# Optimization experiments

Measured on AMD Instinct MI355X. Metric: run time of the kernel, lower is better.

The kernel has to match this reference:

```python
import jax, jax.numpy as jnp
import numpy as np

HEADS = 16
D_MODEL = 1024
D_EXP = 2048  # d_model * expansion_factor
D_HEAD = D_EXP // HEADS
DEPTH = 12
B, L = 2, 2048


def setup_inputs() -> dict:
    key = jax.random.key(0)
    ks = jax.random.split(key, 4)
    x = jax.random.normal(ks[0], (B, L, D_MODEL), dtype=jnp.float32)
    w_in = jax.random.normal(ks[1], (4 * D_EXP, D_MODEL), dtype=jnp.float32) * 0.02
    w_out = jax.random.normal(ks[2], (D_MODEL, D_EXP), dtype=jnp.float32) * (0.02 / np.sqrt(2 * DEPTH))
    # LearnedALiBi init: logspace(0,-6,heads//2,base=2) ++ zeros(heads - heads//2)
    half = HEADS // 2
    slopes = jnp.concatenate([
        jnp.asarray(2.0 ** np.linspace(0.0, -6.0, half), dtype=jnp.float32),
        jnp.zeros((HEADS - half,), dtype=jnp.float32),
    ])
    smear_factor = jnp.linspace(-6.0, 6.0, HEADS, dtype=jnp.float32)
    return {
        "x": x, "w_in": w_in, "w_out": w_out,
        "ln_in_g": jnp.ones((D_MODEL,), jnp.float32), "ln_in_b": jnp.zeros((D_MODEL,), jnp.float32),
        "ln_out_g": jnp.ones((D_MODEL,), jnp.float32), "ln_out_b": jnp.zeros((D_MODEL,), jnp.float32),
        "slopes": slopes, "smear_factor": smear_factor,
    }


def _layernorm(x, g, b, eps=1e-5):
    mu = jnp.mean(x, axis=-1, keepdims=True)
    var = jnp.mean(jnp.square(x - mu), axis=-1, keepdims=True)
    return (x - mu) * jax.lax.rsqrt(var + eps) * g + b


def reference(x, w_in, w_out, ln_in_g, ln_in_b, ln_out_g, ln_out_b, slopes, smear_factor):
    b, l, d = x.shape
    h = _layernorm(x, ln_in_g, ln_in_b)
    qkvp = h @ w_in.T  # (b, l, 4*D_EXP)
    q, k, v, p = jnp.split(qkvp, 4, axis=-1)

    def to_heads(t):  # b i (h d) -> b h i d
        return t.reshape(b, l, HEADS, D_HEAD).transpose(0, 2, 1, 3)

    q, k, v = to_heads(q), to_heads(k), to_heads(v)

    # key smearing: k_i <- (1-s)*k_i + s*k_{i-1}
    smear = jax.nn.sigmoid(smear_factor)[None, :, None, None]
    k_shift = jnp.pad(k, ((0, 0), (0, 0), (1, 0), (0, 0)))[:, :, :-1]
    k = (1.0 - smear) * k + smear * k_shift

    logits = jnp.einsum('bhid,bhjd->bhij', q, k) * (D_HEAD ** -0.5)
    # learned ALiBi bias: j * slope_h  (depends only on key index)
    alibi = jnp.arange(l, dtype=logits.dtype)[None, None, None, :] * slopes[None, :, None, None]
    # causal bias: -1e10 * (1 - tril)
    i_idx = jnp.arange(l)
    causal = jnp.where(i_idx[:, None] >= i_idx[None, :], 0.0, -1e10)[None, None]
    a = jax.nn.softmax(logits + alibi + causal, axis=-1)

    o = jnp.einsum('bhij,bhjd->bhid', a, v)
    o = o.transpose(0, 2, 1, 3).reshape(b, l, D_EXP)  # b h i d -> b i (h d)
    gated = jax.nn.silu(p) * o
    y = gated @ w_out.T
    return _layernorm(y, ln_out_g, ln_out_b)
```

## Files before the change

kernel.cpp:

```cpp
#include <hip/hip_runtime.h>
#include <hip/hip_bf16.h>
#include <stdint.h>


typedef __bf16 bf16;
typedef bf16  bf16x8 __attribute__((ext_vector_type(8)));
typedef bf16  bf16x4 __attribute__((ext_vector_type(4)));
typedef float f32x4  __attribute__((ext_vector_type(4)));

#define SEQ   2048
#define NBATC 2

__device__ __forceinline__ void gld_lds16(const bf16* g, bf16* l) {
  __builtin_amdgcn_global_load_lds((const __attribute__((address_space(1))) void*)g,
                                   (__attribute__((address_space(3))) void*)l, 16, 0, 0);
}

__global__ __launch_bounds__(256) void cvt_kernel(const float* __restrict__ in,
                                                  bf16* __restrict__ out, int n8) {
  int t = blockIdx.x * 256 + threadIdx.x;
  if (t >= n8) return;
  const float4* p = (const float4*)in + (size_t)t * 2;
  float4 a = p[0], b = p[1];
  bf16x8 o;
  o[0] = (bf16)a.x; o[1] = (bf16)a.y; o[2] = (bf16)a.z; o[3] = (bf16)a.w;
  o[4] = (bf16)b.x; o[5] = (bf16)b.y; o[6] = (bf16)b.z; o[7] = (bf16)b.w;
  *((bf16x8*)out + t) = o;
}

template<bool BF16OUT>
__global__ __launch_bounds__(256) void ln_kernel(const float* __restrict__ x,
    const float* __restrict__ gamma, const float* __restrict__ beta,
    void* __restrict__ out) {
  const int row = blockIdx.x;
  const int tid = threadIdx.x;
  float4 v = *(const float4*)(x + (size_t)row * 1024 + tid * 4);
  float s  = v.x + v.y + v.z + v.w;
  float ss = v.x * v.x + v.y * v.y + v.z * v.z + v.w * v.w;
#pragma unroll
  for (int m = 1; m < 64; m <<= 1) { s += __shfl_xor(s, m, 64); ss += __shfl_xor(ss, m, 64); }
  __shared__ float red[8];
  if ((tid & 63) == 0) { red[tid >> 6] = s; red[(tid >> 6) + 4] = ss; }
  __syncthreads();
  s  = red[0] + red[1] + red[2] + red[3];
  ss = red[4] + red[5] + red[6] + red[7];
  const float mu  = s * (1.f / 1024.f);
  const float inv = rsqrtf(ss * (1.f / 1024.f) - mu * mu + 1e-5f);
  float4 g  = *(const float4*)(gamma + tid * 4);
  float4 bb = *(const float4*)(beta  + tid * 4);
  float y0 = (v.x - mu) * inv * g.x + bb.x;
  float y1 = (v.y - mu) * inv * g.y + bb.y;
  float y2 = (v.z - mu) * inv * g.z + bb.z;
  float y3 = (v.w - mu) * inv * g.w + bb.w;
  if (BF16OUT) {
    bf16* o = (bf16*)out + (size_t)row * 1024 + tid * 4;
    o[0] = (bf16)y0; o[1] = (bf16)y1; o[2] = (bf16)y2; o[3] = (bf16)y3;
  } else {
    float* o = (float*)out + (size_t)row * 1024 + tid * 4;
    o[0] = y0; o[1] = y1; o[2] = y2; o[3] = y3;
  }
}

__global__ __launch_bounds__(256) void prep_kernel(const bf16* __restrict__ qkvp,
    const float* __restrict__ smf, bf16* __restrict__ ksm, bf16* __restrict__ vt) {
  __shared__ bf16 T[128][72];
  const int kt = blockIdx.x, bh = blockIdx.y;
  const int b = bh >> 4, h = bh & 15;
  const int t = threadIdx.x;

  {
    int i = t >> 2, d0 = (t & 3) * 32;
    const bf16* src = qkvp + (size_t)(b * SEQ + kt * 64 + i) * 8192 + 4096 + h * 128 + d0;
#pragma unroll
    for (int m = 0; m < 4; m++) {
      bf16x8 v8 = *(const bf16x8*)(src + m * 8);
#pragma unroll
      for (int e = 0; e < 8; e++) T[d0 + m * 8 + e][i] = v8[e];
    }
  }

  {
    float sm = 1.f / (1.f + __expf(-smf[h]));
#pragma unroll
    for (int j = 0; j < 4; j++) {
      int c  = j * 256 + t;
      int il = c >> 4, d8 = c & 15;
      int i  = kt * 64 + il;
      const bf16* base = qkvp + (size_t)(b * SEQ + i) * 8192 + 2048 + h * 128 + d8 * 8;
      bf16x8 cur = *(const bf16x8*)base;
      bf16x8 prv = cur;
      if (i > 0) prv = *(const bf16x8*)(base - 8192);
      bf16x8 o;
#pragma unroll
      for (int e = 0; e < 8; e++) {
        float pv = (i > 0) ? (float)prv[e] : 0.f;
        o[e] = (bf16)((1.f - sm) * (float)cur[e] + sm * pv);
      }
      size_t idx = ((size_t)bh * SEQ + i) * 128 + ((d8 * 8) ^ ((i & 7) << 3));
      *(bf16x8*)(ksm + idx) = o;
    }
  }

  __syncthreads();
  {
    int d = t >> 1, i0 = (t & 1) * 32;
    bf16* dst = vt + (size_t)bh * (SEQ * 128) + (size_t)kt * 8192 + d * 64;
#pragma unroll
    for (int m = 0; m < 4; m++) {
      bf16x8 v8 = *(const bf16x8*)&T[d][i0 + m * 8];
      *(bf16x8*)(dst + (((i0 + m * 8)) ^ ((d & 7) << 3))) = v8;
    }
  }
}

__global__ __launch_bounds__(1024, 4) void gemm256(const bf16* __restrict__ A,
    const bf16* __restrict__ Bt, bf16* __restrict__ C, int M, int N, int K,
    int RX, int SX, int SY) {
  __shared__ bf16 As[2][256 * 64];
  __shared__ bf16 Bs[2][256 * 64];
  const int w   = blockIdx.x;
  const int xcd = w & 7, idx = w >> 3;
  const int rx = xcd % RX, ry = xcd / RX;
  const int bx = rx * SX + idx % SX;
  const int by = ry * SY + idx / SX;
  const int tid  = threadIdx.x;
  const int lane = tid & 63, wid = tid >> 6;
  const int l4 = lane >> 4, l16 = lane & 15;
  const int wr = wid >> 2, wc = wid & 3;
  const int rowBase = by * 256, colBase = bx * 256;
  const int NT = K >> 6;

  f32x4 acc[4][4];
  const f32x4 z = {0.f, 0.f, 0.f, 0.f};
#pragma unroll
  for (int i = 0; i < 4; i++)
#pragma unroll
    for (int j = 0; j < 4; j++) acc[i][j] = z;

  auto stage = [&](int t_, int buf) {
    const int k0 = t_ * 64;
#pragma unroll
    for (int j = 0; j < 2; ++j) {
      const int c   = j * 1024 + tid;
      const int row = c >> 3;
      const int sc  = ((c & 7) * 8) ^ ((row & 7) << 3);
      gld_lds16(A  + (size_t)(rowBase + row) * K + k0 + sc, &As[buf][c * 8]);
      gld_lds16(Bt + (size_t)(colBase + row) * K + k0 + sc, &Bs[buf][c * 8]);
    }
  };

  stage(0, 0);
  for (int t = 0; t < NT; ++t) {
    const int cur = t & 1;
    if (t + 1 < NT) {
      stage(t + 1, cur ^ 1);
      asm volatile("s_waitcnt vmcnt(4)" ::: "memory");
    } else {
      asm volatile("s_waitcnt vmcnt(0)" ::: "memory");
    }
    __builtin_amdgcn_sched_barrier(0);
    __builtin_amdgcn_s_barrier();
    const bf16* a_ = &As[cur][0];
    const bf16* b_ = &Bs[cur][0];
#pragma unroll
    for (int ks = 0; ks < 2; ++ks) {
      bf16x8 bfr[4];
#pragma unroll
      for (int ni = 0; ni < 4; ++ni) {
        const int br = wc * 64 + ni * 16 + l16;
        bfr[ni] = *(const bf16x8*)&b_[br * 64 + ((ks * 32 + l4 * 8) ^ ((br & 7) << 3))];
      }
#pragma unroll
      for (int mi = 0; mi < 4; ++mi) {
        const int ar = wr * 64 + mi * 16 + l16;
        bf16x8 af = *(const bf16x8*)&a_[ar * 64 + ((ks * 32 + l4 * 8) ^ ((ar & 7) << 3))];
#pragma unroll
        for (int ni = 0; ni < 4; ++ni)
          acc[mi][ni] = __builtin_amdgcn_mfma_f32_16x16x32_bf16(af, bfr[ni], acc[mi][ni], 0, 0, 0);
      }
    }
    asm volatile("s_waitcnt lgkmcnt(0)" ::: "memory");
    __builtin_amdgcn_s_barrier();
  }

#pragma unroll
  for (int mi = 0; mi < 4; ++mi)
#pragma unroll
    for (int ni = 0; ni < 4; ++ni) {
      int row = rowBase + wr * 64 + mi * 16 + l4 * 4;
      int col = colBase + wc * 64 + ni * 16 + l16;
#pragma unroll
      for (int r = 0; r < 4; ++r)
        C[(size_t)(row + r) * N + col] = (bf16)acc[mi][ni][r];
    }
}

__global__ __launch_bounds__(256, 2) void gemm128(const bf16* __restrict__ A,
    const bf16* __restrict__ Bt, float* __restrict__ C, int M, int N, int K,
    int RX, int SX, int SY) {
  __shared__ bf16 As[2][128 * 64];
  __shared__ bf16 Bs[2][128 * 64];
  const int w   = blockIdx.x;
  const int xcd = w & 7, idx = w >> 3;
  const int rx = xcd % RX, ry = xcd / RX;
  const int bx = rx * SX + idx % SX;
  const int by = ry * SY + idx / SX;
  const int tid  = threadIdx.x;
  const int lane = tid & 63, wid = tid >> 6;
  const int l4 = lane >> 4, l16 = lane & 15;
  const int wr = wid >> 1, wc = wid & 1;
  const int rowBase = by * 128, colBase = bx * 128;
  const int NT = K >> 6;

  f32x4 acc[4][4];
  const f32x4 z = {0.f, 0.f, 0.f, 0.f};
#pragma unroll
  for (int i = 0; i < 4; i++)
#pragma unroll
    for (int j = 0; j < 4; j++) acc[i][j] = z;

  auto stage = [&](int t_, int buf) {
    const int k0 = t_ * 64;
#pragma unroll
    for (int j = 0; j < 4; ++j) {
      const int c   = j * 256 + tid;
      const int row = c >> 3;
      const int sc  = ((c & 7) * 8) ^ ((row & 7) << 3);
      gld_lds16(A  + (size_t)(rowBase + row) * K + k0 + sc, &As[buf][c * 8]);
      gld_lds16(Bt + (size_t)(colBase + row) * K + k0 + sc, &Bs[buf][c * 8]);
    }
  };

  stage(0, 0);
  for (int t = 0; t < NT; ++t) {
    const int cur = t & 1;
    if (t + 1 < NT) {
      stage(t + 1, cur ^ 1);
      asm volatile("s_waitcnt vmcnt(8)" ::: "memory");
    } else {
      asm volatile("s_waitcnt vmcnt(0)" ::: "memory");
    }
    __builtin_amdgcn_sched_barrier(0);
    __builtin_amdgcn_s_barrier();
    const bf16* a_ = &As[cur][0];
    const bf16* b_ = &Bs[cur][0];
#pragma unroll
    for (int ks = 0; ks < 2; ++ks) {
      bf16x8 bfr[4];
#pragma unroll
      for (int ni = 0; ni < 4; ++ni) {
        const int br = wc * 64 + ni * 16 + l16;
        bfr[ni] = *(const bf16x8*)&b_[br * 64 + ((ks * 32 + l4 * 8) ^ ((br & 7) << 3))];
      }
#pragma unroll
      for (int mi = 0; mi < 4; ++mi) {
        const int ar = wr * 64 + mi * 16 + l16;
        bf16x8 af = *(const bf16x8*)&a_[ar * 64 + ((ks * 32 + l4 * 8) ^ ((ar & 7) << 3))];
#pragma unroll
        for (int ni = 0; ni < 4; ++ni)
          acc[mi][ni] = __builtin_amdgcn_mfma_f32_16x16x32_bf16(af, bfr[ni], acc[mi][ni], 0, 0, 0);
      }
    }
    asm volatile("s_waitcnt lgkmcnt(0)" ::: "memory");
    __builtin_amdgcn_s_barrier();
  }

#pragma unroll
  for (int mi = 0; mi < 4; ++mi)
#pragma unroll
    for (int ni = 0; ni < 4; ++ni) {
      int row = rowBase + wr * 64 + mi * 16 + l4 * 4;
      int col = colBase + wc * 64 + ni * 16 + l16;
#pragma unroll
      for (int r = 0; r < 4; ++r)
        C[(size_t)(row + r) * N + col] = acc[mi][ni][r];
    }
}

__global__ __launch_bounds__(512, 2) void attn_kernel(const bf16* __restrict__ qkvp,
    const bf16* __restrict__ ksm, const bf16* __restrict__ vt,
    const float* __restrict__ slopes, bf16* __restrict__ gated) {
  const int w   = blockIdx.x;
  const int xcd = w & 7;
  const int bh  = xcd * 4 + ((w >> 3) & 3);
  const int pr  = w >> 5;
  const int b   = bh >> 4, h = bh & 15;
  const int tid = threadIdx.x, wid = tid >> 6, lane = tid & 63;
  const int l4 = lane >> 4, l16 = lane & 15;
  const int swz = (l16 & 7) << 3;
  const float LOG2E = 1.44269504f;
  const float s2 = 0.08838834764831845f * LOG2E;
  const float slopeL = slopes[h] * LOG2E;

  __shared__ bf16 Kb[4][64 * 128];
  __shared__ bf16 Vb[4][64 * 128];
  __shared__ bf16 P_lds[128 * 64];

  const bf16* ksmB = ksm + (size_t)bh * SEQ * 128;
  const bf16* vtB  = vt  + (size_t)bh * SEQ * 128;

  auto stage = [&](int kt, int bsel) {
#pragma unroll
    for (int j = 0; j < 2; j++) {
      const int c = j * 512 + tid;
      gld_lds16(ksmB + (size_t)kt * 8192 + c * 8, &Kb[bsel][c * 8]);
      gld_lds16(vtB  + (size_t)kt * 8192 + c * 8, &Vb[bsel][c * 8]);
    }
  };

  auto run_strip = [&](int qtile) {
    const int nt = 2 * qtile + 2;
    int kt0 = 0;
    if (slopeL > 1e-6f) {
      const int W = (int)(64.f / slopeL + 128.f);
      const int wlim = qtile * 128 - W - 63;
      if (wlim > 0) kt0 = (wlim >> 6) & ~1;
    }
    const int iq = qtile * 128 + wid * 16 + l16;
    bf16x8 qf[4];
    {
      const bf16* qrow = qkvp + (size_t)(b * SEQ + iq) * 8192 + h * 128;
#pragma unroll
      for (int kb = 0; kb < 4; kb++) qf[kb] = *(const bf16x8*)(qrow + kb * 32 + l4 * 8);
    }
    f32x4 oacc[8];
    const f32x4 z = {0.f, 0.f, 0.f, 0.f};
#pragma unroll
    for (int i = 0; i < 8; i++) oacc[i] = z;
    float m2 = -1e38f, lpart = 0.f;

    auto tile = [&](int t, const bf16* K_, const bf16* V_) {
      f32x4 sacc[4];
#pragma unroll
      for (int jf = 0; jf < 4; jf++) {
        f32x4 a = z;
#pragma unroll
        for (int kb = 0; kb < 4; kb++) {
          bf16x8 kf = *(const bf16x8*)&K_[(jf * 16 + l16) * 128 + ((kb * 32 + l4 * 8) ^ swz)];
          a = __builtin_amdgcn_mfma_f32_16x16x32_bf16(kf, qf[kb], a, 0, 0, 0);
        }
        sacc[jf] = a;
      }

      const bool diag = (t >= 2 * qtile);
      const int kbase = t * 64 + l4 * 4;
#pragma unroll
      for (int jf = 0; jf < 4; jf++) {
#pragma unroll
        for (int r = 0; r < 4; r++) {
          int j = kbase + jf * 16 + r;
          float v = fmaf(sacc[jf][r], s2, (float)j * slopeL);
          if (diag && j > iq) v = -1e38f;
          sacc[jf][r] = v;
        }
      }

      float mx = sacc[0][0];
#pragma unroll
      for (int jf = 0; jf < 4; jf++)
#pragma unroll
        for (int r = 0; r < 4; r++) mx = fmaxf(mx, sacc[jf][r]);
      mx = fmaxf(mx, __shfl_xor(mx, 16, 64));
      mx = fmaxf(mx, __shfl_xor(mx, 32, 64));

      if (__any(mx > m2 + 14.f)) {
        float mnew  = fmaxf(m2, mx);
        float alpha = __builtin_amdgcn_exp2f(m2 - mnew);
        m2 = mnew;
        lpart *= alpha;
#pragma unroll
        for (int df = 0; df < 8; df++) oacc[df] *= alpha;
      }

      float rs = 0.f;
#pragma unroll
      for (int jf = 0; jf < 4; jf++) {
        bf16x4 pw;
#pragma unroll
        for (int r = 0; r < 4; r++) {
          float pe = __builtin_amdgcn_exp2f(sacc[jf][r] - m2);
          rs += pe;
          pw[r] = (bf16)pe;
        }
        *(bf16x4*)&P_lds[(wid * 16 + l16) * 64 + ((jf * 16 + l4 * 4) ^ swz)] = pw;
      }
      lpart += rs;

#pragma unroll
      for (int kb2 = 0; kb2 < 2; ++kb2) {
        bf16x8 pf = *(const bf16x8*)&P_lds[(wid * 16 + l16) * 64 + ((kb2 * 32 + l4 * 8) ^ swz)];
#pragma unroll
        for (int df = 0; df < 8; df++) {
          bf16x8 vf = *(const bf16x8*)&V_[(df * 16 + l16) * 64 + ((kb2 * 32 + l4 * 8) ^ swz)];
          oacc[df] = __builtin_amdgcn_mfma_f32_16x16x32_bf16(vf, pf, oacc[df], 0, 0, 0);
        }
      }
    };

    stage(kt0, kt0 & 3);
    stage(kt0 + 1, (kt0 + 1) & 3);
    for (int tp = kt0; tp < nt; tp += 2) {
      if (tp + 2 < nt) {
        stage(tp + 2, (tp + 2) & 3);
        stage(tp + 3, (tp + 3) & 3);
        asm volatile("s_waitcnt vmcnt(8)" ::: "memory");
      } else {
        asm volatile("s_waitcnt vmcnt(0)" ::: "memory");
      }
      __builtin_amdgcn_sched_barrier(0);
      __builtin_amdgcn_s_barrier();
      tile(tp,     Kb[tp & 3],       Vb[tp & 3]);
      tile(tp + 1, Kb[(tp + 1) & 3], Vb[(tp + 1) & 3]);
      asm volatile("s_waitcnt lgkmcnt(0)" ::: "memory");
      __builtin_amdgcn_s_barrier();
    }

    lpart += __shfl_xor(lpart, 16, 64);
    lpart += __shfl_xor(lpart, 32, 64);
    const float linv = 1.f / lpart;
    const bf16* pgrow = qkvp + (size_t)(b * SEQ + iq) * 8192 + 6144 + h * 128;
    bf16* grow = gated + (size_t)(b * SEQ + iq) * 2048 + h * 128;
#pragma unroll
    for (int df = 0; df < 8; df++) {
      const int d0 = df * 16 + l4 * 4;
      bf16x4 pg4 = *(const bf16x4*)(pgrow + d0);
      bf16x4 o4;
#pragma unroll
      for (int r = 0; r < 4; r++) {
        float o  = oacc[df][r] * linv;
        float pg = (float)pg4[r];
        float silu = pg / (1.f + __expf(-pg));
        o4[r] = (bf16)(silu * o);
      }
      *(bf16x4*)(grow + d0) = o4;
    }
  };

  run_strip(15 - pr);
  run_strip(pr);
}

extern "C" void kernel_launch(void* const* d_in, const int* in_sizes, int n_in,
                              void* d_out, int out_size, void* d_ws, size_t ws_size,
                              hipStream_t stream) {
  (void)in_sizes; (void)n_in; (void)out_size; (void)ws_size;
  const float* x      = (const float*)d_in[0];
  const float* w_in   = (const float*)d_in[1];
  const float* w_out  = (const float*)d_in[2];
  const float* lnig   = (const float*)d_in[3];
  const float* lnib   = (const float*)d_in[4];
  const float* lnog   = (const float*)d_in[5];
  const float* lnob   = (const float*)d_in[6];
  const float* slopes = (const float*)d_in[7];
  const float* smf    = (const float*)d_in[8];
  float* out = (float*)d_out;

  char* ws = (char*)d_ws;
  size_t off = 0;
  bf16* hb      = (bf16*)(ws + off); off += (size_t)4096 * 1024 * 2;
  bf16* w_in_b  = (bf16*)(ws + off); off += (size_t)8192 * 1024 * 2;
  bf16* w_out_b = (bf16*)(ws + off); off += (size_t)1024 * 2048 * 2;
  bf16* qkvp    = (bf16*)(ws + off); off += (size_t)4096 * 8192 * 2;
  bf16* ksm     = (bf16*)(ws + off); off += (size_t)32 * 2048 * 128 * 2;
  bf16* gated   = (bf16*)(ws + off); off += (size_t)4096 * 2048 * 2;
  float* yb     = (float*)(ws + off); off += (size_t)4096 * 1024 * 4;
  bf16* vt      = (bf16*)yb;

  cvt_kernel<<<4096, 256, 0, stream>>>(w_in,  w_in_b,  8388608 / 8);
  cvt_kernel<<<1024, 256, 0, stream>>>(w_out, w_out_b, 2097152 / 8);
  ln_kernel<true><<<4096, 256, 0, stream>>>(x, lnig, lnib, hb);
  gemm256<<<512, 1024, 0, stream>>>(hb, w_in_b, qkvp, 4096, 8192, 1024, 4, 8, 8);
  prep_kernel<<<dim3(32, 32), 256, 0, stream>>>(qkvp, smf, ksm, vt);
  attn_kernel<<<256, 512, 0, stream>>>(qkvp, ksm, vt, slopes, gated);
  gemm128<<<256, 256, 0, stream>>>(gated, w_out_b, yb, 4096, 1024, 2048, 1, 8, 4);
  ln_kernel<false><<<4096, 256, 0, stream>>>(yb, lnog, lnob, out);
}
```

Baseline: 218.0 us.

## Split attention strips into separate blocks with smaller LDS for higher occupancy

Each block now handles one query strip instead of two paired strips, so the grid doubles to 512 blocks. K/V staging drops from four buffers with two-tile steps to a double buffer with one tile per step, and the P scratch is halved and reused for two 32-column halves. Less shared memory and launch_bounds(512,4) are meant to let more blocks share a CU and hide latency. In exchange, per-block load balance from pairing long and short strips is lost, and the single-tile pipeline has a shallower prefetch and more barriers.

```diff
diff --git a/kernel.cpp b/kernel.cpp
--- a/kernel.cpp
+++ b/kernel.cpp
@@ -277,24 +277,25 @@
     }
 }
 
-__global__ __launch_bounds__(512, 2) void attn_kernel(const bf16* __restrict__ qkvp,
+__global__ __launch_bounds__(512, 4) void attn_kernel(const bf16* __restrict__ qkvp,
     const bf16* __restrict__ ksm, const bf16* __restrict__ vt,
     const float* __restrict__ slopes, bf16* __restrict__ gated) {
   const int w   = blockIdx.x;
-  const int xcd = w & 7;
-  const int bh  = xcd * 4 + ((w >> 3) & 3);
-  const int pr  = w >> 5;
+  const int bh  = (w & 7) * 4 + ((w >> 3) & 3);
+  const int pr  = (w >> 5) & 7;
+  const int qtile = (w >> 8) ? pr : 15 - pr;
   const int b   = bh >> 4, h = bh & 15;
   const int tid = threadIdx.x, wid = tid >> 6, lane = tid & 63;
   const int l4 = lane >> 4, l16 = lane & 15;
-  const int swz = (l16 & 7) << 3;
+  const int swz  = (l16 & 7) << 3;
+  const int swzP = (l16 & 3) << 3;
   const float LOG2E = 1.44269504f;
   const float s2 = 0.08838834764831845f * LOG2E;
   const float slopeL = slopes[h] * LOG2E;
 
-  __shared__ bf16 Kb[4][64 * 128];
-  __shared__ bf16 Vb[4][64 * 128];
-  __shared__ bf16 P_lds[128 * 64];
+  __shared__ bf16 Kb[2][64 * 128];
+  __shared__ bf16 Vb[2][64 * 128];
+  __shared__ bf16 P8[128 * 32];
 
   const bf16* ksmB = ksm + (size_t)bh * SEQ * 128;
   const bf16* vtB  = vt  + (size_t)bh * SEQ * 128;
@@ -308,136 +309,142 @@
     }
   };
 
-  auto run_strip = [&](int qtile) {
-    const int nt = 2 * qtile + 2;
-    int kt0 = 0;
-    if (slopeL > 1e-6f) {
-      const int W = (int)(64.f / slopeL + 128.f);
-      const int wlim = qtile * 128 - W - 63;
-      if (wlim > 0) kt0 = (wlim >> 6) & ~1;
-    }
-    const int iq = qtile * 128 + wid * 16 + l16;
-    bf16x8 qf[4];
+  const int nt = 2 * qtile + 2;
+  int kt0 = 0;
+  if (slopeL > 1e-6f) {
+    const int W = (int)(64.f / slopeL + 128.f);
+    const int wlim = qtile * 128 - W - 63;
+    if (wlim > 0) kt0 = wlim >> 6;
+  }
+
+  const int iq = qtile * 128 + wid * 16 + l16;
+  bf16x8 qf[4];
+  {
+    const bf16* qrow = qkvp + (size_t)(b * SEQ + iq) * 8192 + h * 128;
+#pragma unroll
+    for (int kb = 0; kb < 4; kb++) qf[kb] = *(const bf16x8*)(qrow + kb * 32 + l4 * 8);
+  }
+  f32x4 oacc[8];
+  const f32x4 z = {0.f, 0.f, 0.f, 0.f};
+#pragma unroll
+  for (int i = 0; i < 8; i++) oacc[i] = z;
+  float m2 = -1e38f, lpart = 0.f;
+
+  const int prow = (wid * 16 + l16) * 32;
+
+  stage(kt0, kt0 & 1);
+  for (int t = kt0; t < nt; ++t) {
+    const int cur = t & 1;
+    if (t + 1 < nt) {
+      stage(t + 1, cur ^ 1);
+      asm volatile("s_waitcnt vmcnt(4)" ::: "memory");
+    } else {
+      asm volatile("s_waitcnt vmcnt(0)" ::: "memory");
+    }
+    __builtin_amdgcn_sched_barrier(0);
+    __builtin_amdgcn_s_barrier();
+    const bf16* K_ = Kb[cur];
+    const bf16* V_ = Vb[cur];
+
+    f32x4 sacc[4];
+#pragma unroll
+    for (int jf = 0; jf < 4; jf++) {
+      f32x4 a = z;
+#pragma unroll
+      for (int kb = 0; kb < 4; kb++) {
+        bf16x8 kf = *(const bf16x8*)&K_[(jf * 16 + l16) * 128 + ((kb * 32 + l4 * 8) ^ swz)];
+        a = __builtin_amdgcn_mfma_f32_16x16x32_bf16(kf, qf[kb], a, 0, 0, 0);
+      }
+      sacc[jf] = a;
+    }
+
+    const bool diag = (t >= 2 * qtile);
+    const int kbase = t * 64 + l4 * 4;
+#pragma unroll
+    for (int jf = 0; jf < 4; jf++) {
+#pragma unroll
+      for (int r = 0; r < 4; r++) {
+        int j = kbase + jf * 16 + r;
+        float v = fmaf(sacc[jf][r], s2, (float)j * slopeL);
+        if (diag && j > iq) v = -1e38f;
+        sacc[jf][r] = v;
+      }
+    }
+
+    float mx = sacc[0][0];
+#pragma unroll
+    for (int jf = 0; jf < 4; jf++)
+#pragma unroll
+      for (int r = 0; r < 4; r++) mx = fmaxf(mx, sacc[jf][r]);
+    mx = fmaxf(mx, __shfl_xor(mx, 16, 64));
+    mx = fmaxf(mx, __shfl_xor(mx, 32, 64));
+
+    if (__any(mx > m2 + 14.f)) {
+      float mnew  = fmaxf(m2, mx);
+      float alpha = __builtin_amdgcn_exp2f(m2 - mnew);
+      m2 = mnew;
+      lpart *= alpha;
+#pragma unroll
+      for (int df = 0; df < 8; df++) oacc[df] *= alpha;
+    }
+
+    bf16x4 pw[4];
+    float rs = 0.f;
+#pragma unroll
+    for (int jf = 0; jf < 4; jf++) {
+#pragma unroll
+      for (int r = 0; r < 4; r++) {
+        float pe = __builtin_amdgcn_exp2f(sacc[jf][r] - m2);
+        rs += pe;
+        pw[jf][r] = (bf16)pe;
+      }
+    }
+    lpart += rs;
+
+    *(bf16x4*)&P8[prow + ((l4 * 4) ^ swzP)]      = pw[0];
+    *(bf16x4*)&P8[prow + ((16 + l4 * 4) ^ swzP)] = pw[1];
     {
-      const bf16* qrow = qkvp + (size_t)(b * SEQ + iq) * 8192 + h * 128;
-#pragma unroll
-      for (int kb = 0; kb < 4; kb++) qf[kb] = *(const bf16x8*)(qrow + kb * 32 + l4 * 8);
-    }
-    f32x4 oacc[8];
-    const f32x4 z = {0.f, 0.f, 0.f, 0.f};
-#pragma unroll
-    for (int i = 0; i < 8; i++) oacc[i] = z;
-    float m2 = -1e38f, lpart = 0.f;
-
-    auto tile = [&](int t, const bf16* K_, const bf16* V_) {
-      f32x4 sacc[4];
-#pragma unroll
-      for (int jf = 0; jf < 4; jf++) {
-        f32x4 a = z;
-#pragma unroll
-        for (int kb = 0; kb < 4; kb++) {
-          bf16x8 kf = *(const bf16x8*)&K_[(jf * 16 + l16) * 128 + ((kb * 32 + l4 * 8) ^ swz)];
-          a = __builtin_amdgcn_mfma_f32_16x16x32_bf16(kf, qf[kb], a, 0, 0, 0);
-        }
-        sacc[jf] = a;
-      }
-
-      const bool diag = (t >= 2 * qtile);
-      const int kbase = t * 64 + l4 * 4;
-#pragma unroll
-      for (int jf = 0; jf < 4; jf++) {
-#pragma unroll
-        for (int r = 0; r < 4; r++) {
-          int j = kbase + jf * 16 + r;
-          float v = fmaf(sacc[jf][r], s2, (float)j * slopeL);
-          if (diag && j > iq) v = -1e38f;
-          sacc[jf][r] = v;
-        }
-      }
-
-      float mx = sacc[0][0];
-#pragma unroll
-      for (int jf = 0; jf < 4; jf++)
-#pragma unroll
-        for (int r = 0; r < 4; r++) mx = fmaxf(mx, sacc[jf][r]);
-      mx = fmaxf(mx, __shfl_xor(mx, 16, 64));
-      mx = fmaxf(mx, __shfl_xor(mx, 32, 64));
-
-      if (__any(mx > m2 + 14.f)) {
-        float mnew  = fmaxf(m2, mx);
-        float alpha = __builtin_amdgcn_exp2f(m2 - mnew);
-        m2 = mnew;
-        lpart *= alpha;
-#pragma unroll
-        for (int df = 0; df < 8; df++) oacc[df] *= alpha;
-      }
-
-      float rs = 0.f;
-#pragma unroll
-      for (int jf = 0; jf < 4; jf++) {
-        bf16x4 pw;
-#pragma unroll
-        for (int r = 0; r < 4; r++) {
-          float pe = __builtin_amdgcn_exp2f(sacc[jf][r] - m2);
-          rs += pe;
-          pw[r] = (bf16)pe;
-        }
-        *(bf16x4*)&P_lds[(wid * 16 + l16) * 64 + ((jf * 16 + l4 * 4) ^ swz)] = pw;
-      }
-      lpart += rs;
-
-#pragma unroll
-      for (int kb2 = 0; kb2 < 2; ++kb2) {
-        bf16x8 pf = *(const bf16x8*)&P_lds[(wid * 16 + l16) * 64 + ((kb2 * 32 + l4 * 8) ^ swz)];
-#pragma unroll
-        for (int df = 0; df < 8; df++) {
-          bf16x8 vf = *(const bf16x8*)&V_[(df * 16 + l16) * 64 + ((kb2 * 32 + l4 * 8) ^ swz)];
-          oacc[df] = __builtin_amdgcn_mfma_f32_16x16x32_bf16(vf, pf, oacc[df], 0, 0, 0);
-        }
-      }
-    };
-
-    stage(kt0, kt0 & 3);
-    stage(kt0 + 1, (kt0 + 1) & 3);
-    for (int tp = kt0; tp < nt; tp += 2) {
-      if (tp + 2 < nt) {
-        stage(tp + 2, (tp + 2) & 3);
-        stage(tp + 3, (tp + 3) & 3);
-        asm volatile("s_waitcnt vmcnt(8)" ::: "memory");
-      } else {
-        asm volatile("s_waitcnt vmcnt(0)" ::: "memory");
-      }
-      __builtin_amdgcn_sched_barrier(0);
-      __builtin_amdgcn_s_barrier();
-      tile(tp,     Kb[tp & 3],       Vb[tp & 3]);
-      tile(tp + 1, Kb[(tp + 1) & 3], Vb[(tp + 1) & 3]);
-      asm volatile("s_waitcnt lgkmcnt(0)" ::: "memory");
-      __builtin_amdgcn_s_barrier();
-    }
-
-    lpart += __shfl_xor(lpart, 16, 64);
-    lpart += __shfl_xor(lpart, 32, 64);
-    const float linv = 1.f / lpart;
-    const bf16* pgrow = qkvp + (size_t)(b * SEQ + iq) * 8192 + 6144 + h * 128;
-    bf16* grow = gated + (size_t)(b * SEQ + iq) * 2048 + h * 128;
-#pragma unroll
-    for (int df = 0; df < 8; df++) {
-      const int d0 = df * 16 + l4 * 4;
-      bf16x4 pg4 = *(const bf16x4*)(pgrow + d0);
-      bf16x4 o4;
-#pragma unroll
-      for (int r = 0; r < 4; r++) {
-        float o  = oacc[df][r] * linv;
-        float pg = (float)pg4[r];
-        float silu = pg / (1.f + __expf(-pg));
-        o4[r] = (bf16)(silu * o);
-      }
-      *(bf16x4*)(grow + d0) = o4;
-    }
-  };
-
-  run_strip(15 - pr);
-  run_strip(pr);
+      bf16x8 pf = *(const bf16x8*)&P8[prow + ((l4 * 8) ^ swzP)];
+#pragma unroll
+      for (int df = 0; df < 8; df++) {
+        bf16x8 vf = *(const bf16x8*)&V_[(df * 16 + l16) * 64 + ((l4 * 8) ^ swz)];
+        oacc[df] = __builtin_amdgcn_mfma_f32_16x16x32_bf16(vf, pf, oacc[df], 0, 0, 0);
+      }
+    }
+    *(bf16x4*)&P8[prow + ((l4 * 4) ^ swzP)]      = pw[2];
+    *(bf16x4*)&P8[prow + ((16 + l4 * 4) ^ swzP)] = pw[3];
+    {
+      bf16x8 pf = *(const bf16x8*)&P8[prow + ((l4 * 8) ^ swzP)];
+#pragma unroll
+      for (int df = 0; df < 8; df++) {
+        bf16x8 vf = *(const bf16x8*)&V_[(df * 16 + l16) * 64 + ((32 + l4 * 8) ^ swz)];
+        oacc[df] = __builtin_amdgcn_mfma_f32_16x16x32_bf16(vf, pf, oacc[df], 0, 0, 0);
+      }
+    }
+
+    asm volatile("s_waitcnt lgkmcnt(0)" ::: "memory");
+    __builtin_amdgcn_s_barrier();
+  }
+
+  lpart += __shfl_xor(lpart, 16, 64);
+  lpart += __shfl_xor(lpart, 32, 64);
+  const float linv = 1.f / lpart;
+  const bf16* pgrow = qkvp + (size_t)(b * SEQ + iq) * 8192 + 6144 + h * 128;
+  bf16* grow = gated + (size_t)(b * SEQ + iq) * 2048 + h * 128;
+#pragma unroll
+  for (int df = 0; df < 8; df++) {
+    const int d0 = df * 16 + l4 * 4;
+    bf16x4 pg4 = *(const bf16x4*)(pgrow + d0);
+    bf16x4 o4;
+#pragma unroll
+    for (int r = 0; r < 4; r++) {
+      float o  = oacc[df][r] * linv;
+      float pg = (float)pg4[r];
+      float silu = pg / (1.f + __expf(-pg));
+      o4[r] = (bf16)(silu * o);
+    }
+    *(bf16x4*)(grow + d0) = o4;
+  }
 }
 
 extern "C" void kernel_launch(void* const* d_in, const int* in_sizes, int n_in,
@@ -471,7 +478,7 @@
   ln_kernel<true><<<4096, 256, 0, stream>>>(x, lnig, lnib, hb);
   gemm256<<<512, 1024, 0, stream>>>(hb, w_in_b, qkvp, 4096, 8192, 1024, 4, 8, 8);
   prep_kernel<<<dim3(32, 32), 256, 0, stream>>>(qkvp, smf, ksm, vt);
-  attn_kernel<<<256, 512, 0, stream>>>(qkvp, ksm, vt, slopes, gated);
+  attn_kernel<<<512, 512, 0, stream>>>(qkvp, ksm, vt, slopes, gated);
   gemm128<<<256, 256, 0, stream>>>(gated, w_out_b, yb, 4096, 1024, 2048, 1, 8, 4);
   ln_kernel<false><<<4096, 256, 0, stream>>>(yb, lnog, lnob, out);
 }
```

After: 223.9 us. +2.7%, slower.
